# Kernel tuning notes

Hardware: AMD Instinct MI355X
Metric: run time of the kernel (lower is better)

## Reference

```python
import jax, jax.numpy as jnp
import numpy as np


def setup_inputs() -> dict:
    key = jax.random.key(0)
    k1, k2, k3 = jax.random.split(key, 3)
    B, E, L, D = 32, 256, 2048, 256
    doc_state = jax.random.normal(k1, (B, L, D), dtype=jnp.float32)
    entity_mapping = jax.random.uniform(k2, (B, E, L), dtype=jnp.float32)
    entity_lens = jax.random.uniform(k3, (B, E), dtype=jnp.float32)
    return {"doc_state": doc_state, "entity_mapping": entity_mapping, "entity_lens": entity_lens}


def reference(doc_state, entity_mapping, entity_lens):
    # Original: (entity_mapping[:, :, :, None] * doc_state[:, None, :, :]).sum(2) / entity_lens[:, :, None]
    # This is a batched contraction over L; express as einsum to avoid the
    # huge [B, E, L, D] intermediate.
    summed = jnp.einsum('bel,bld->bed', entity_mapping, doc_state)  # [B, E, D]
    return summed / entity_lens[:, :, None]
```

## Files before the change

kernel.cpp:

```cpp
#include <hip/hip_runtime.h>
#include <stdint.h>

#define B_ 32
#define E_ 256
#define L_ 2048
#define D_ 256

#define BE 64
#define BD 128
#define BK 64
#define KS 4
#define KCHUNK (L_ / KS)
#define NKT (KCHUNK / BK)

typedef __attribute__((ext_vector_type(2))) float  f32x2;
typedef __attribute__((ext_vector_type(4))) float  f32x4;
typedef __attribute__((ext_vector_type(4))) short  s16x4;
typedef __attribute__((ext_vector_type(8))) short  s16x8;

__device__ __forceinline__ void cvt_hilo1(float x, short &h, short &l) {
    unsigned u = __builtin_bit_cast(unsigned, x);
    h = (short)(u >> 16);
    float hf = __builtin_bit_cast(float, u & 0xFFFF0000u);
    unsigned r = __builtin_bit_cast(unsigned, x - hf);
    l = (short)(r >> 16);
}
__device__ __forceinline__ void cvt_hilo4(const f32x4 v, s16x4 &h, s16x4 &l) {
    #pragma unroll
    for (int i = 0; i < 4; ++i) { short hh, ll; cvt_hilo1(v[i], hh, ll); h[i] = hh; l[i] = ll; }
}

__global__ void zero_out_kernel(f32x4* __restrict__ out) {
    out[(size_t)blockIdx.x * 256 + threadIdx.x] = f32x4{0.f, 0.f, 0.f, 0.f};
}

__global__ __launch_bounds__(512, 6)
void mean_pool_kernel(const float* __restrict__ doc,
                      const float* __restrict__ emap,
                      const float* __restrict__ lens,
                      float* __restrict__ out) {
    __shared__ __align__(16) short As_hi[BE][BK];
    __shared__ __align__(16) short As_lo[BE][BK];
    __shared__ __align__(16) short Bs_hi[BD][BK];
    __shared__ __align__(16) short Bs_lo[BD][BK];
    __shared__ float lens_s[BE];

    const int t   = threadIdx.x;
    const int blk = blockIdx.x;
    const int ks  = blk & 3;
    const int d0  = ((blk >> 2) & 1) * BD;
    const int e0  = ((blk >> 3) & 3) * BE;
    const int b   = blk >> 5;

    const float* Ag = emap + ((size_t)b * E_ + e0) * L_ + ks * KCHUNK;
    const float* Sg = doc  + (size_t)b * L_ * D_ + (size_t)ks * KCHUNK * D_ + d0;

    if (t < BE) lens_s[t] = lens[b * E_ + e0 + t];

    const int a_c4 = t & 15;
    const int a_r  = t >> 4;
    const int db = t & 63;
    const int kb = t >> 6;

    const int lane = t & 63;
    const int w    = t >> 6;
    const int eo   = (w & 1) * 32;
    const int dq   = (w >> 1) * 32;
    const int ml   = lane & 15;
    const int kg   = lane >> 4;

    f32x4 acc[2][2] = {};
    f32x4 pa[2];
    f32x2 pb[8];

    #pragma unroll
    for (int rr = 0; rr < 2; ++rr)
        pa[rr] = *(const f32x4*)(Ag + (size_t)(a_r + rr * 32) * L_ + a_c4 * 4);
    #pragma unroll
    for (int i = 0; i < 8; ++i)
        pb[i] = *(const f32x2*)(Sg + (size_t)(kb * 8 + i) * D_ + db * 2);

    for (int kt = 0; kt < NKT; ++kt) {
        #pragma unroll
        for (int rr = 0; rr < 2; ++rr) {
            const int row = a_r + rr * 32;
            s16x4 h, l;
            cvt_hilo4(pa[rr], h, l);
            const int col = (((a_c4 >> 1) ^ (row & 7)) << 3) + (a_c4 & 1) * 4;
            *(s16x4*)&As_hi[row][col] = h;
            *(s16x4*)&As_lo[row][col] = l;
        }
        #pragma unroll
        for (int dd = 0; dd < 2; ++dd) {
            const int row = db * 2 + dd;
            s16x8 h, l;
            #pragma unroll
            for (int j = 0; j < 8; ++j) {
                short hh, ll; cvt_hilo1(pb[j][dd], hh, ll);
                h[j] = hh; l[j] = ll;
            }
            const int key = (db & 3) | (((db >> 2) & 1) << 2);
            const int col = (kb ^ key) << 3;
            *(s16x8*)&Bs_hi[row][col] = h;
            *(s16x8*)&Bs_lo[row][col] = l;
        }
        __syncthreads();

        if (kt + 1 < NKT) {
            const int k0 = (kt + 1) * BK;
            #pragma unroll
            for (int rr = 0; rr < 2; ++rr)
                pa[rr] = *(const f32x4*)(Ag + (size_t)(a_r + rr * 32) * L_ + k0 + a_c4 * 4);
            #pragma unroll
            for (int i = 0; i < 8; ++i)
                pb[i] = *(const f32x2*)(Sg + (size_t)(k0 + kb * 8 + i) * D_ + db * 2);
        }

        #pragma unroll
        for (int kc = 0; kc < 2; ++kc) {
            const int gbase = kc * 4;
            s16x8 ah[2], al[2], bh[2], bl[2];
            #pragma unroll
            for (int mi = 0; mi < 2; ++mi) {
                const int row = eo + mi * 16 + ml;
                const int col = ((gbase + kg) ^ (row & 7)) << 3;
                ah[mi] = *(const s16x8*)&As_hi[row][col];
                al[mi] = *(const s16x8*)&As_lo[row][col];
            }
            #pragma unroll
            for (int ni = 0; ni < 2; ++ni) {
                const int row = dq + ni * 16 + ml;
                const int keyB = ((row >> 1) & 3) | (((row >> 3) & 1) << 2);
                const int col  = ((gbase + kg) ^ keyB) << 3;
                bh[ni] = *(const s16x8*)&Bs_hi[row][col];
                bl[ni] = *(const s16x8*)&Bs_lo[row][col];
            }
            #pragma unroll
            for (int mi = 0; mi < 2; ++mi)
                #pragma unroll
                for (int ni = 0; ni < 2; ++ni) {
                    acc[mi][ni] = __builtin_amdgcn_mfma_f32_16x16x32_bf16(ah[mi], bh[ni], acc[mi][ni], 0, 0, 0);
                    acc[mi][ni] = __builtin_amdgcn_mfma_f32_16x16x32_bf16(ah[mi], bl[ni], acc[mi][ni], 0, 0, 0);
                    acc[mi][ni] = __builtin_amdgcn_mfma_f32_16x16x32_bf16(al[mi], bh[ni], acc[mi][ni], 0, 0, 0);
                }
        }
        __syncthreads();
    }

    #pragma unroll
    for (int mi = 0; mi < 2; ++mi) {
        #pragma unroll
        for (int rr = 0; rr < 4; ++rr) {
            const int er = eo + mi * 16 + kg * 4 + rr;
            const float lv = lens_s[er];
            #pragma unroll
            for (int ni = 0; ni < 2; ++ni) {
                atomicAdd(&out[((size_t)(b * E_ + e0 + er)) * D_ + d0 + dq + ni * 16 + ml],
                          acc[mi][ni][rr] / lv);
            }
        }
    }
}

extern "C" void kernel_launch(void* const* d_in, const int* in_sizes, int n_in,
                              void* d_out, int out_size, void* d_ws, size_t ws_size,
                              hipStream_t stream) {
    const float* doc  = (const float*)d_in[0];
    const float* emap = (const float*)d_in[1];
    const float* lens = (const float*)d_in[2];
    float* out = (float*)d_out;

    zero_out_kernel<<<dim3(out_size / (4 * 256)), dim3(256), 0, stream>>>((f32x4*)out);

    dim3 grid(B_ * (E_ / BE) * (D_ / BD) * KS);
    dim3 block(512);
    hipLaunchKernelGGL(mean_pool_kernel, grid, block, 0, stream,
                       doc, emap, lens, out);
}
```

Measured before the change: 173.2 us.

## Halve K tile to 32 and remap loaders for higher occupancy

Shrinks the K tile from 64 to 32, so each thread now loads one f32x4 of the entity map and eight scalar doc values per tile instead of twice as many. The shared-memory swizzles and loader thread mapping are rewritten for the narrower tile, and launch bounds are raised to 8 blocks per CU. The aim is to cut register and LDS footprint so more workgroups are resident and latency is better hidden. The cost is twice as many K iterations and barriers, plus narrower scalar global loads for the doc tensor.

```diff
diff --git a/kernel.cpp b/kernel.cpp
--- a/kernel.cpp
+++ b/kernel.cpp
@@ -8,12 +8,11 @@
 
 #define BE 64
 #define BD 128
-#define BK 64
+#define BK 32
 #define KS 4
 #define KCHUNK (L_ / KS)
 #define NKT (KCHUNK / BK)
 
-typedef __attribute__((ext_vector_type(2))) float  f32x2;
 typedef __attribute__((ext_vector_type(4))) float  f32x4;
 typedef __attribute__((ext_vector_type(4))) short  s16x4;
 typedef __attribute__((ext_vector_type(8))) short  s16x8;
@@ -25,16 +24,12 @@
     unsigned r = __builtin_bit_cast(unsigned, x - hf);
     l = (short)(r >> 16);
 }
-__device__ __forceinline__ void cvt_hilo4(const f32x4 v, s16x4 &h, s16x4 &l) {
-    #pragma unroll
-    for (int i = 0; i < 4; ++i) { short hh, ll; cvt_hilo1(v[i], hh, ll); h[i] = hh; l[i] = ll; }
-}
 
 __global__ void zero_out_kernel(f32x4* __restrict__ out) {
     out[(size_t)blockIdx.x * 256 + threadIdx.x] = f32x4{0.f, 0.f, 0.f, 0.f};
 }
 
-__global__ __launch_bounds__(512, 6)
+__global__ __launch_bounds__(512, 8)
 void mean_pool_kernel(const float* __restrict__ doc,
                       const float* __restrict__ emap,
                       const float* __restrict__ lens,
@@ -57,10 +52,10 @@
 
     if (t < BE) lens_s[t] = lens[b * E_ + e0 + t];
 
-    const int a_c4 = t & 15;
-    const int a_r  = t >> 4;
-    const int db = t & 63;
-    const int kb = t >> 6;
+    const int a_c4 = t & 7;
+    const int a_r  = t >> 3;
+    const int b_d  = t & 127;
+    const int b_g  = t >> 7;
 
     const int lane = t & 63;
     const int w    = t >> 6;
@@ -70,68 +65,57 @@
     const int kg   = lane >> 4;
 
     f32x4 acc[2][2] = {};
-    f32x4 pa[2];
-    f32x2 pb[8];
+    f32x4 pa;
+    float pb[8];
 
+    pa = *(const f32x4*)(Ag + (size_t)a_r * L_ + a_c4 * 4);
     #pragma unroll
-    for (int rr = 0; rr < 2; ++rr)
-        pa[rr] = *(const f32x4*)(Ag + (size_t)(a_r + rr * 32) * L_ + a_c4 * 4);
-    #pragma unroll
-    for (int i = 0; i < 8; ++i)
-        pb[i] = *(const f32x2*)(Sg + (size_t)(kb * 8 + i) * D_ + db * 2);
+    for (int j = 0; j < 8; ++j)
+        pb[j] = Sg[(size_t)(b_g * 8 + j) * D_ + b_d];
 
     for (int kt = 0; kt < NKT; ++kt) {
-        #pragma unroll
-        for (int rr = 0; rr < 2; ++rr) {
-            const int row = a_r + rr * 32;
+        {
             s16x4 h, l;
-            cvt_hilo4(pa[rr], h, l);
-            const int col = (((a_c4 >> 1) ^ (row & 7)) << 3) + (a_c4 & 1) * 4;
-            *(s16x4*)&As_hi[row][col] = h;
-            *(s16x4*)&As_lo[row][col] = l;
+            #pragma unroll
+            for (int i = 0; i < 4; ++i) { short hh, ll; cvt_hilo1(pa[i], hh, ll); h[i] = hh; l[i] = ll; }
+            const int col = (((a_c4 >> 1) ^ (a_r & 3)) << 3) + (a_c4 & 1) * 4;
+            *(s16x4*)&As_hi[a_r][col] = h;
+            *(s16x4*)&As_lo[a_r][col] = l;
         }
-        #pragma unroll
-        for (int dd = 0; dd < 2; ++dd) {
-            const int row = db * 2 + dd;
+        {
             s16x8 h, l;
             #pragma unroll
             for (int j = 0; j < 8; ++j) {
-                short hh, ll; cvt_hilo1(pb[j][dd], hh, ll);
+                short hh, ll; cvt_hilo1(pb[j], hh, ll);
                 h[j] = hh; l[j] = ll;
             }
-            const int key = (db & 3) | (((db >> 2) & 1) << 2);
-            const int col = (kb ^ key) << 3;
-            *(s16x8*)&Bs_hi[row][col] = h;
-            *(s16x8*)&Bs_lo[row][col] = l;
+            const int col = (b_g ^ ((b_d >> 1) & 3)) << 3;
+            *(s16x8*)&Bs_hi[b_d][col] = h;
+            *(s16x8*)&Bs_lo[b_d][col] = l;
         }
         __syncthreads();
 
         if (kt + 1 < NKT) {
             const int k0 = (kt + 1) * BK;
+            pa = *(const f32x4*)(Ag + (size_t)a_r * L_ + k0 + a_c4 * 4);
             #pragma unroll
-            for (int rr = 0; rr < 2; ++rr)
-                pa[rr] = *(const f32x4*)(Ag + (size_t)(a_r + rr * 32) * L_ + k0 + a_c4 * 4);
-            #pragma unroll
-            for (int i = 0; i < 8; ++i)
-                pb[i] = *(const f32x2*)(Sg + (size_t)(k0 + kb * 8 + i) * D_ + db * 2);
+            for (int j = 0; j < 8; ++j)
+                pb[j] = Sg[(size_t)(k0 + b_g * 8 + j) * D_ + b_d];
         }
 
-        #pragma unroll
-        for (int kc = 0; kc < 2; ++kc) {
-            const int gbase = kc * 4;
+        {
             s16x8 ah[2], al[2], bh[2], bl[2];
             #pragma unroll
             for (int mi = 0; mi < 2; ++mi) {
                 const int row = eo + mi * 16 + ml;
-                const int col = ((gbase + kg) ^ (row & 7)) << 3;
+                const int col = (kg ^ (row & 3)) << 3;
                 ah[mi] = *(const s16x8*)&As_hi[row][col];
                 al[mi] = *(const s16x8*)&As_lo[row][col];
             }
             #pragma unroll
             for (int ni = 0; ni < 2; ++ni) {
                 const int row = dq + ni * 16 + ml;
-                const int keyB = ((row >> 1) & 3) | (((row >> 3) & 1) << 2);
-                const int col  = ((gbase + kg) ^ keyB) << 3;
+                const int col = (kg ^ ((row >> 1) & 3)) << 3;
                 bh[ni] = *(const s16x8*)&Bs_hi[row][col];
                 bl[ni] = *(const s16x8*)&Bs_lo[row][col];
             }
```

Measured after the change: 176.1 us. Within noise of the previous version (+1.6%).
